# Kernel optimization log

Measured on AMD Instinct MI355X. Metric: run time of the kernel, lower is better.

Reference implementation:

```python
import jax, jax.numpy as jnp
import numpy as np

N = 100000      # nodes
E = 1600000     # edges
D_IN, D_H, D_OUT = 256, 64, 47


def setup_inputs() -> dict:
    key = jax.random.key(0)
    k0, k1, k2, k3 = jax.random.split(key, 4)
    x = jax.random.normal(k0, (N, D_IN), dtype=jnp.float32)
    edge_index = jax.random.randint(k1, (2, E), 0, N, dtype=jnp.int64)
    W1 = jax.random.normal(k2, (D_IN, D_H), dtype=jnp.float32) / np.sqrt(D_IN)
    b1 = jnp.zeros((D_H,), dtype=jnp.float32)
    W2 = jax.random.normal(k3, (D_H, D_OUT), dtype=jnp.float32) / np.sqrt(D_H)
    b2 = jnp.zeros((D_OUT,), dtype=jnp.float32)
    return {"x": x, "edge_index": edge_index, "W1": W1, "b1": b1, "W2": W2, "b2": b2}


def _gcn_conv(x, W, b, src, dst, norm):
    # PyG GCNConv: h = x @ W, then scatter_add(norm * h[src] -> dst), + bias
    h = x @ W                                     # [N, out]
    msg = norm[:, None] * h[src]                  # [E+N, out] gather
    out = jax.ops.segment_sum(msg, dst, num_segments=N)  # scatter-add
    return out + b


def reference(x, edge_index, W1, b1, W2, b2):
    # add self-loops with weight 1 (PyG default, edge_weight=None -> ones)
    loop = jnp.arange(N, dtype=edge_index.dtype)
    src = jnp.concatenate([edge_index[0], loop])
    dst = jnp.concatenate([edge_index[1], loop])
    w = jnp.ones((E + N,), dtype=x.dtype)
    # symmetric normalization: deg^-1/2[src] * w * deg^-1/2[dst]
    deg = jax.ops.segment_sum(w, dst, num_segments=N)
    dinv = jnp.where(deg > 0, jax.lax.rsqrt(deg), 0.0)
    norm = dinv[src] * w * dinv[dst]              # [E+N]

    h = _gcn_conv(x, W1, b1, src, dst, norm)
    h = jax.nn.relu(h)
    # F.dropout(training=self.training): eval mode -> identity
    xo = _gcn_conv(h, W2, b2, src, dst, norm)     # [N, D_OUT]
    logits = jax.nn.softmax(xo, axis=1)           # nn.Softmax() -> dim=1 for 2D
    preds = jnp.argmax(logits, axis=1)
    return (logits, preds, xo)
```

## Files before the change

kernel.cpp:

```cpp
#include <hip/hip_runtime.h>
#include <math.h>

#define NN 100000
#define NE 1600000
#define DI 256
#define DH 64
#define DO 47
#define DH3 48
#define PAD 48
#define RSZ8 ((NN + 7) / 8)
#define EPB 2048
#define CPB ((NE + EPB - 1) / EPB)

__global__ __launch_bounds__(256) void k_fill1(const int* __restrict__ src,
                                               const int* __restrict__ dst,
                                               int* __restrict__ deg,
                                               int* __restrict__ csr_pad) {
    int r = blockIdx.x & 7;
    int chunk = blockIdx.x >> 3;
    int lo = r * RSZ8, hi = min(lo + RSZ8, NN);
    int base = chunk * EPB + threadIdx.x;
    int dv[8];
    #pragma unroll
    for (int i = 0; i < 8; ++i) {
        int e = base + i * 256;
        dv[i] = (e < NE) ? __builtin_nontemporal_load(dst + e) : -1;
    }
    #pragma unroll
    for (int i = 0; i < 8; ++i) {
        int d = dv[i];
        if (d >= lo && d < hi) {
            int e = base + i * 256;
            int s = __builtin_nontemporal_load(src + e);
            int p = atomicAdd(&deg[d], 1);
            if (p < PAD) csr_pad[d * PAD + p] = s;
        }
    }
}

__global__ __launch_bounds__(512) void k_gemm1(const float* __restrict__ x,
                                               const float* __restrict__ W1,
                                               const int* __restrict__ deg,
                                               float* __restrict__ h1s) {
    __shared__ float xs[2][128 * 33];
    __shared__ float wl[2][32 * 64];
    const int t = threadIdx.x;
    const int lane = t & 63;
    const int wvu = __builtin_amdgcn_readfirstlane(t >> 6);
    const int r0 = blockIdx.x * 128;
    const int sr = t >> 2;
    const int sk = (t & 3) * 8;
    const int wk = t >> 4;
    const int wc = (t & 15) * 4;
    const long xrow = (long)min(r0 + sr, NN - 1) * DI;
    const int rowA = r0 + lane;
    const int rowB = r0 + 64 + lane;

    float accA[8] = {0.f, 0.f, 0.f, 0.f, 0.f, 0.f, 0.f, 0.f};
    float accB[8] = {0.f, 0.f, 0.f, 0.f, 0.f, 0.f, 0.f, 0.f};

    {
        float4 v0 = *(const float4*)(x + xrow + sk);
        float4 v1 = *(const float4*)(x + xrow + sk + 4);
        float* p = &xs[0][sr * 33 + sk];
        p[0] = v0.x; p[1] = v0.y; p[2] = v0.z; p[3] = v0.w;
        p[4] = v1.x; p[5] = v1.y; p[6] = v1.z; p[7] = v1.w;
        float4 w = *(const float4*)(W1 + (size_t)wk * DH + wc);
        float* q = &wl[0][wk * 64 + wc];
        q[0] = w.x; q[1] = w.y; q[2] = w.z; q[3] = w.w;
    }
    __syncthreads();
    for (int c = 0; c < 8; ++c) {
        const int buf = c & 1;
        if (c + 1 < 8) {
            float4 v0 = *(const float4*)(x + xrow + (c + 1) * 32 + sk);
            float4 v1 = *(const float4*)(x + xrow + (c + 1) * 32 + sk + 4);
            float* p = &xs[buf ^ 1][sr * 33 + sk];
            p[0] = v0.x; p[1] = v0.y; p[2] = v0.z; p[3] = v0.w;
            p[4] = v1.x; p[5] = v1.y; p[6] = v1.z; p[7] = v1.w;
            float4 w = *(const float4*)(W1 + (size_t)((c + 1) * 32 + wk) * DH + wc);
            float* q = &wl[buf ^ 1][wk * 64 + wc];
            q[0] = w.x; q[1] = w.y; q[2] = w.z; q[3] = w.w;
        }
        #pragma unroll 4
        for (int kk = 0; kk < 32; ++kk) {
            float xa = xs[buf][lane * 33 + kk];
            float xb = xs[buf][(lane + 64) * 33 + kk];
            const float4* wp = (const float4*)&wl[buf][kk * 64 + wvu * 8];
            float4 wa = wp[0], wb = wp[1];
            accA[0] += wa.x * xa; accA[1] += wa.y * xa;
            accA[2] += wa.z * xa; accA[3] += wa.w * xa;
            accA[4] += wb.x * xa; accA[5] += wb.y * xa;
            accA[6] += wb.z * xa; accA[7] += wb.w * xa;
            accB[0] += wa.x * xb; accB[1] += wa.y * xb;
            accB[2] += wa.z * xb; accB[3] += wa.w * xb;
            accB[4] += wb.x * xb; accB[5] += wb.y * xb;
            accB[6] += wb.z * xb; accB[7] += wb.w * xb;
        }
        __syncthreads();
    }
    if (rowA < NN) {
        float di = rsqrtf((float)(deg[rowA] + 1));
        float4 o0 = {di * accA[0], di * accA[1], di * accA[2], di * accA[3]};
        float4 o1 = {di * accA[4], di * accA[5], di * accA[6], di * accA[7]};
        float4* hp = (float4*)(h1s + (long)rowA * DH + wvu * 8);
        hp[0] = o0;
        hp[1] = o1;
    }
    if (rowB < NN) {
        float di = rsqrtf((float)(deg[rowB] + 1));
        float4 o0 = {di * accB[0], di * accB[1], di * accB[2], di * accB[3]};
        float4 o1 = {di * accB[4], di * accB[5], di * accB[6], di * accB[7]};
        float4* hp = (float4*)(h1s + (long)rowB * DH + wvu * 8);
        hp[0] = o0;
        hp[1] = o1;
    }
}

__global__ __launch_bounds__(256) void k_agg1(const int* __restrict__ deg,
                                              const int* __restrict__ csr_pad,
                                              const float* __restrict__ h1s,
                                              const float* __restrict__ b1,
                                              const float* __restrict__ W2,
                                              float* __restrict__ h3s) {
    __shared__ float w2[DH * DO];
    __shared__ float sh[8][DH];
    for (int i = threadIdx.x; i < DH * DO; i += 256) w2[i] = W2[i];
    __syncthreads();
    const int wv = threadIdx.x >> 6, lane = threadIdx.x & 63;
    const int c = lane & 15, e = lane >> 4;
    const unsigned c4 = (unsigned)(c * 4);
    const int rA = blockIdx.x * 8 + wv * 2, rB = rA + 1;
    const int degA = deg[rA], degB = deg[rB];
    const int cntA = min(degA, PAD), cntB = min(degB, PAD);
    const unsigned baseA = (unsigned)rA * PAD, baseB = (unsigned)rB * PAD;
    float aAx = 0.f, aAy = 0.f, aAz = 0.f, aAw = 0.f;
    float aBx = 0.f, aBy = 0.f, aBz = 0.f, aBw = 0.f;
    const int cmin = min(cntA, cntB), tmax = max(cntA, cntB);
    int j = 0;
    for (; j + 7 < cmin; j += 8) {
        unsigned sa0 = (unsigned)csr_pad[baseA + j + e];
        unsigned sb0 = (unsigned)csr_pad[baseB + j + e];
        unsigned sa1 = (unsigned)csr_pad[baseA + j + 4 + e];
        unsigned sb1 = (unsigned)csr_pad[baseB + j + 4 + e];
        float4 va0 = *(const float4*)(h1s + sa0 * 64u + c4);
        float4 vb0 = *(const float4*)(h1s + sb0 * 64u + c4);
        float4 va1 = *(const float4*)(h1s + sa1 * 64u + c4);
        float4 vb1 = *(const float4*)(h1s + sb1 * 64u + c4);
        aAx += va0.x + va1.x; aAy += va0.y + va1.y;
        aAz += va0.z + va1.z; aAw += va0.w + va1.w;
        aBx += vb0.x + vb1.x; aBy += vb0.y + vb1.y;
        aBz += vb0.z + vb1.z; aBw += vb0.w + vb1.w;
    }
    for (; j < tmax; j += 4) {
        int slot = min(j + e, PAD - 1);
        unsigned sa = min((unsigned)csr_pad[baseA + slot], (unsigned)(NN - 1));
        unsigned sb = min((unsigned)csr_pad[baseB + slot], (unsigned)(NN - 1));
        float4 va = *(const float4*)(h1s + sa * 64u + c4);
        float4 vb = *(const float4*)(h1s + sb * 64u + c4);
        float mA = (j + e < cntA) ? 1.f : 0.f;
        float mB = (j + e < cntB) ? 1.f : 0.f;
        aAx = fmaf(mA, va.x, aAx); aAy = fmaf(mA, va.y, aAy);
        aAz = fmaf(mA, va.z, aAz); aAw = fmaf(mA, va.w, aAw);
        aBx = fmaf(mB, vb.x, aBx); aBy = fmaf(mB, vb.y, aBy);
        aBz = fmaf(mB, vb.z, aBz); aBw = fmaf(mB, vb.w, aBw);
    }
    aAx += __shfl_xor(aAx, 16); aAx += __shfl_xor(aAx, 32);
    aAy += __shfl_xor(aAy, 16); aAy += __shfl_xor(aAy, 32);
    aAz += __shfl_xor(aAz, 16); aAz += __shfl_xor(aAz, 32);
    aAw += __shfl_xor(aAw, 16); aAw += __shfl_xor(aAw, 32);
    aBx += __shfl_xor(aBx, 16); aBx += __shfl_xor(aBx, 32);
    aBy += __shfl_xor(aBy, 16); aBy += __shfl_xor(aBy, 32);
    aBz += __shfl_xor(aBz, 16); aBz += __shfl_xor(aBz, 32);
    aBw += __shfl_xor(aBw, 16); aBw += __shfl_xor(aBw, 32);
    const float diA = rsqrtf((float)(degA + 1));
    const float diB = rsqrtf((float)(degB + 1));
    if (lane < 16) {
        float4 sA = *(const float4*)(h1s + (unsigned)rA * 64u + c4);
        float4 sB = *(const float4*)(h1s + (unsigned)rB * 64u + c4);
        float4 bb = *(const float4*)(b1 + c4);
        float4 oA, oB;
        oA.x = fmaxf(diA * (aAx + sA.x) + bb.x, 0.f);
        oA.y = fmaxf(diA * (aAy + sA.y) + bb.y, 0.f);
        oA.z = fmaxf(diA * (aAz + sA.z) + bb.z, 0.f);
        oA.w = fmaxf(diA * (aAw + sA.w) + bb.w, 0.f);
        oB.x = fmaxf(diB * (aBx + sB.x) + bb.x, 0.f);
        oB.y = fmaxf(diB * (aBy + sB.y) + bb.y, 0.f);
        oB.z = fmaxf(diB * (aBz + sB.z) + bb.z, 0.f);
        oB.w = fmaxf(diB * (aBw + sB.w) + bb.w, 0.f);
        *(float4*)&sh[wv * 2 + 0][c4] = oA;
        *(float4*)&sh[wv * 2 + 1][c4] = oB;
    }
    __syncthreads();
    if (lane < DO) {
        float oA = 0.f, oB = 0.f;
        #pragma unroll 8
        for (int k = 0; k < DH; ++k) {
            float w = w2[k * DO + lane];
            oA += sh[wv * 2 + 0][k] * w;
            oB += sh[wv * 2 + 1][k] * w;
        }
        h3s[(unsigned)rA * DH3 + lane] = diA * oA;
        h3s[(unsigned)rB * DH3 + lane] = diB * oB;
    }
}

__global__ __launch_bounds__(256) void k_agg2(const int* __restrict__ deg,
                                              const int* __restrict__ csr_pad,
                                              const float* __restrict__ h3s,
                                              const float* __restrict__ b2,
                                              float* __restrict__ logits,
                                              float* __restrict__ preds,
                                              float* __restrict__ xo) {
    const int wv = threadIdx.x >> 6, lane = threadIdx.x & 63;
    const int c = lane & 15, e = lane >> 4;
    const unsigned cc4 = (unsigned)(((c < 12) ? c : 0) * 4);
    const int rA = blockIdx.x * 8 + wv * 2, rB = rA + 1;
    const int degA = deg[rA], degB = deg[rB];
    const int cntA = min(degA, PAD), cntB = min(degB, PAD);
    const unsigned baseA = (unsigned)rA * PAD, baseB = (unsigned)rB * PAD;
    float aAx = 0.f, aAy = 0.f, aAz = 0.f, aAw = 0.f;
    float aBx = 0.f, aBy = 0.f, aBz = 0.f, aBw = 0.f;
    const int cmin = min(cntA, cntB), tmax = max(cntA, cntB);
    int j = 0;
    for (; j + 7 < cmin; j += 8) {
        unsigned sa0 = (unsigned)csr_pad[baseA + j + e];
        unsigned sb0 = (unsigned)csr_pad[baseB + j + e];
        unsigned sa1 = (unsigned)csr_pad[baseA + j + 4 + e];
        unsigned sb1 = (unsigned)csr_pad[baseB + j + 4 + e];
        float4 va0 = *(const float4*)(h3s + sa0 * 48u + cc4);
        float4 vb0 = *(const float4*)(h3s + sb0 * 48u + cc4);
        float4 va1 = *(const float4*)(h3s + sa1 * 48u + cc4);
        float4 vb1 = *(const float4*)(h3s + sb1 * 48u + cc4);
        aAx += va0.x + va1.x; aAy += va0.y + va1.y;
        aAz += va0.z + va1.z; aAw += va0.w + va1.w;
        aBx += vb0.x + vb1.x; aBy += vb0.y + vb1.y;
        aBz += vb0.z + vb1.z; aBw += vb0.w + vb1.w;
    }
    for (; j < tmax; j += 4) {
        int slot = min(j + e, PAD - 1);
        unsigned sa = min((unsigned)csr_pad[baseA + slot], (unsigned)(NN - 1));
        unsigned sb = min((unsigned)csr_pad[baseB + slot], (unsigned)(NN - 1));
        float4 va = *(const float4*)(h3s + sa * 48u + cc4);
        float4 vb = *(const float4*)(h3s + sb * 48u + cc4);
        float mA = (j + e < cntA) ? 1.f : 0.f;
        float mB = (j + e < cntB) ? 1.f : 0.f;
        aAx = fmaf(mA, va.x, aAx); aAy = fmaf(mA, va.y, aAy);
        aAz = fmaf(mA, va.z, aAz); aAw = fmaf(mA, va.w, aAw);
        aBx = fmaf(mB, vb.x, aBx); aBy = fmaf(mB, vb.y, aBy);
        aBz = fmaf(mB, vb.z, aBz); aBw = fmaf(mB, vb.w, aBw);
    }
    aAx += __shfl_xor(aAx, 16); aAx += __shfl_xor(aAx, 32);
    aAy += __shfl_xor(aAy, 16); aAy += __shfl_xor(aAy, 32);
    aAz += __shfl_xor(aAz, 16); aAz += __shfl_xor(aAz, 32);
    aAw += __shfl_xor(aAw, 16); aAw += __shfl_xor(aAw, 32);
    aBx += __shfl_xor(aBx, 16); aBx += __shfl_xor(aBx, 32);
    aBy += __shfl_xor(aBy, 16); aBy += __shfl_xor(aBy, 32);
    aBz += __shfl_xor(aBz, 16); aBz += __shfl_xor(aBz, 32);
    aBw += __shfl_xor(aBw, 16); aBw += __shfl_xor(aBw, 32);
    const float diA = rsqrtf((float)(degA + 1));
    const float diB = rsqrtf((float)(degB + 1));
    const bool lv = (lane < 16) && (c < 12);
    float b0 = 0.f, bq1 = 0.f, bq2 = 0.f, bq3 = 0.f;
    if (lv) {
        b0 = b2[c * 4 + 0]; bq1 = b2[c * 4 + 1]; bq2 = b2[c * 4 + 2];
        bq3 = (c < 11) ? b2[c * 4 + 3] : 0.f;
    }
    #pragma unroll
    for (int rr = 0; rr < 2; ++rr) {
        const int row = rr ? rB : rA;
        const float di = rr ? diB : diA;
        float ax = rr ? aBx : aAx, ay = rr ? aBy : aAy;
        float az = rr ? aBz : aAz, aw = rr ? aBw : aAw;
        float vx = -INFINITY, vy = -INFINITY, vz = -INFINITY, vw = -INFINITY;
        if (lv) {
            float4 sf = *(const float4*)(h3s + (unsigned)row * 48u + cc4);
            vx = di * (ax + sf.x) + b0;
            vy = di * (ay + sf.y) + bq1;
            vz = di * (az + sf.z) + bq2;
            vw = (c < 11) ? (di * (aw + sf.w) + bq3) : -INFINITY;
            float* xp = xo + (size_t)row * DO + c * 4;
            xp[0] = vx; xp[1] = vy; xp[2] = vz;
            if (c < 11) xp[3] = vw;
        }
        float lm = fmaxf(fmaxf(vx, vy), fmaxf(vz, vw));
        float gm = lm;
        for (int off = 32; off; off >>= 1) gm = fmaxf(gm, __shfl_xor(gm, off));
        int cand = 1 << 30;
        if (lv) {
            if (vx == gm) cand = c * 4 + 0;
            else if (vy == gm) cand = c * 4 + 1;
            else if (vz == gm) cand = c * 4 + 2;
            else if (c < 11 && vw == gm) cand = c * 4 + 3;
        }
        for (int off = 32; off; off >>= 1) cand = min(cand, __shfl_xor(cand, off));
        float e0 = 0.f, e1 = 0.f, e2 = 0.f, e3 = 0.f;
        if (lv) {
            e0 = expf(vx - gm); e1 = expf(vy - gm); e2 = expf(vz - gm);
            e3 = (c < 11) ? expf(vw - gm) : 0.f;
        }
        float gs = e0 + e1 + e2 + e3;
        for (int off = 32; off; off >>= 1) gs += __shfl_xor(gs, off);
        if (lv) {
            float* lp = logits + (size_t)row * DO + c * 4;
            lp[0] = e0 / gs; lp[1] = e1 / gs; lp[2] = e2 / gs;
            if (c < 11) lp[3] = e3 / gs;
        }
        if (lane == 0) preds[row] = (float)cand;
    }
}

extern "C" void kernel_launch(void* const* d_in, const int* in_sizes, int n_in,
                              void* d_out, int out_size, void* d_ws, size_t ws_size,
                              hipStream_t stream) {
    const float* x  = (const float*)d_in[0];
    const int*   ei = (const int*)d_in[1];
    const float* W1 = (const float*)d_in[2];
    const float* b1 = (const float*)d_in[3];
    const float* W2 = (const float*)d_in[4];
    const float* b2 = (const float*)d_in[5];
    const int* src = ei;
    const int* dst = ei + NE;

    float* out    = (float*)d_out;
    float* logits = out;
    float* preds  = out + (size_t)NN * DO;
    float* xo     = preds + NN;

    char* wsb = (char*)d_ws;
    int*   deg     = (int*)wsb;                         wsb += (size_t)NN * 4;
    int*   csr_pad = (int*)wsb;                         wsb += (size_t)NN * PAD * 4;
    float* h1s     = (float*)wsb;                       wsb += (size_t)NN * DH * 4;
    float* h3s     = (float*)wsb;                       wsb += (size_t)NN * DH3 * 4;

    hipMemsetAsync(deg, 0, NN * sizeof(int), stream);

    k_fill1<<<8 * CPB, 256, 0, stream>>>(src, dst, deg, csr_pad);
    k_gemm1<<<(NN + 127) / 128, 512, 0, stream>>>(x, W1, deg, h1s);
    k_agg1<<<NN / 8, 256, 0, stream>>>(deg, csr_pad, h1s, b1, W2, h3s);
    k_agg2<<<NN / 8, 256, 0, stream>>>(deg, csr_pad, h3s, b2, logits, preds, xo);
}
```

Before: 298.3 us.

## Fuse CSR fill with first GEMM in one interleaved launch; defer degree scaling

```diff
diff --git a/kernel.cpp b/kernel.cpp
--- a/kernel.cpp
+++ b/kernel.cpp
@@ -11,43 +11,51 @@
 #define RSZ8 ((NN + 7) / 8)
 #define EPB 2048
 #define CPB ((NE + EPB - 1) / EPB)
-
-__global__ __launch_bounds__(256) void k_fill1(const int* __restrict__ src,
+#define GNB ((NN + 127) / 128)
+#define FNB (GNB * 9)
+
+__global__ __launch_bounds__(512) void k_fused(const int* __restrict__ src,
                                                const int* __restrict__ dst,
+                                               const float* __restrict__ x,
+                                               const float* __restrict__ W1,
                                                int* __restrict__ deg,
-                                               int* __restrict__ csr_pad) {
-    int r = blockIdx.x & 7;
-    int chunk = blockIdx.x >> 3;
-    int lo = r * RSZ8, hi = min(lo + RSZ8, NN);
-    int base = chunk * EPB + threadIdx.x;
-    int dv[8];
-    #pragma unroll
-    for (int i = 0; i < 8; ++i) {
-        int e = base + i * 256;
-        dv[i] = (e < NE) ? __builtin_nontemporal_load(dst + e) : -1;
-    }
-    #pragma unroll
-    for (int i = 0; i < 8; ++i) {
-        int d = dv[i];
-        if (d >= lo && d < hi) {
-            int e = base + i * 256;
-            int s = __builtin_nontemporal_load(src + e);
-            int p = atomicAdd(&deg[d], 1);
-            if (p < PAD) csr_pad[d * PAD + p] = s;
-        }
-    }
-}
-
-__global__ __launch_bounds__(512) void k_gemm1(const float* __restrict__ x,
-                                               const float* __restrict__ W1,
-                                               const int* __restrict__ deg,
-                                               float* __restrict__ h1s) {
+                                               int* __restrict__ csr_pad,
+                                               float* __restrict__ h1u) {
     __shared__ float xs[2][128 * 33];
     __shared__ float wl[2][32 * 64];
+    const int b = blockIdx.x;
     const int t = threadIdx.x;
+
+    if (b % 9 != 0) {
+        const int r = b & 7;
+        const int k = ((b % 72) - r) >> 3;
+        const int ordinal = k - (k > r ? 1 : 0);
+        const int chunk = (b / 72) * 8 + ordinal;
+        const int lo = r * RSZ8, hi = min(lo + RSZ8, NN);
+        const int base = chunk * EPB + t;
+        int dv[4];
+        #pragma unroll
+        for (int i = 0; i < 4; ++i) {
+            int e = base + i * 512;
+            dv[i] = (e < NE) ? __builtin_nontemporal_load(dst + e) : -1;
+        }
+        #pragma unroll
+        for (int i = 0; i < 4; ++i) {
+            int d = dv[i];
+            if (d >= lo && d < hi) {
+                int e = base + i * 512;
+                int s = __builtin_nontemporal_load(src + e);
+                int p = atomicAdd(&deg[d], 1);
+                if (p < PAD) csr_pad[d * PAD + p] = s;
+            }
+        }
+        return;
+    }
+
+    const int g = b / 9;
     const int lane = t & 63;
     const int wvu = __builtin_amdgcn_readfirstlane(t >> 6);
-    const int r0 = blockIdx.x * 128;
+    const int r0 = g * 128;
     const int sr = t >> 2;
     const int sk = (t & 3) * 8;
     const int wk = t >> 4;
@@ -100,26 +108,31 @@
         __syncthreads();
     }
     if (rowA < NN) {
-        float di = rsqrtf((float)(deg[rowA] + 1));
-        float4 o0 = {di * accA[0], di * accA[1], di * accA[2], di * accA[3]};
-        float4 o1 = {di * accA[4], di * accA[5], di * accA[6], di * accA[7]};
-        float4* hp = (float4*)(h1s + (long)rowA * DH + wvu * 8);
+        float4 o0 = {accA[0], accA[1], accA[2], accA[3]};
+        float4 o1 = {accA[4], accA[5], accA[6], accA[7]};
+        float4* hp = (float4*)(h1u + (long)rowA * DH + wvu * 8);
         hp[0] = o0;
         hp[1] = o1;
     }
     if (rowB < NN) {
-        float di = rsqrtf((float)(deg[rowB] + 1));
-        float4 o0 = {di * accB[0], di * accB[1], di * accB[2], di * accB[3]};
-        float4 o1 = {di * accB[4], di * accB[5], di * accB[6], di * accB[7]};
-        float4* hp = (float4*)(h1s + (long)rowB * DH + wvu * 8);
+        float4 o0 = {accB[0], accB[1], accB[2], accB[3]};
+        float4 o1 = {accB[4], accB[5], accB[6], accB[7]};
+        float4* hp = (float4*)(h1u + (long)rowB * DH + wvu * 8);
         hp[0] = o0;
         hp[1] = o1;
     }
 }
 
+__global__ __launch_bounds__(256) void k_dinv(const int* __restrict__ deg,
+                                              float* __restrict__ dinv) {
+    int i = blockIdx.x * 256 + threadIdx.x;
+    if (i < NN) dinv[i] = rsqrtf((float)(deg[i] + 1));
+}
+
 __global__ __launch_bounds__(256) void k_agg1(const int* __restrict__ deg,
+                                              const float* __restrict__ dinv,
                                               const int* __restrict__ csr_pad,
-                                              const float* __restrict__ h1s,
+                                              const float* __restrict__ h1u,
                                               const float* __restrict__ b1,
                                               const float* __restrict__ W2,
                                               float* __restrict__ h3s) {
@@ -131,8 +144,7 @@
     const int c = lane & 15, e = lane >> 4;
     const unsigned c4 = (unsigned)(c * 4);
     const int rA = blockIdx.x * 8 + wv * 2, rB = rA + 1;
-    const int degA = deg[rA], degB = deg[rB];
-    const int cntA = min(degA, PAD), cntB = min(degB, PAD);
+    const int cntA = min(deg[rA], PAD), cntB = min(deg[rB], PAD);
     const unsigned baseA = (unsigned)rA * PAD, baseB = (unsigned)rB * PAD;
     float aAx = 0.f, aAy = 0.f, aAz = 0.f, aAw = 0.f;
     float aBx = 0.f, aBy = 0.f, aBz = 0.f, aBw = 0.f;
@@ -143,27 +155,32 @@
         unsigned sb0 = (unsigned)csr_pad[baseB + j + e];
         unsigned sa1 = (unsigned)csr_pad[baseA + j + 4 + e];
         unsigned sb1 = (unsigned)csr_pad[baseB + j + 4 + e];
-        float4 va0 = *(const float4*)(h1s + sa0 * 64u + c4);
-        float4 vb0 = *(const float4*)(h1s + sb0 * 64u + c4);
-        float4 va1 = *(const float4*)(h1s + sa1 * 64u + c4);
-        float4 vb1 = *(const float4*)(h1s + sb1 * 64u + c4);
-        aAx += va0.x + va1.x; aAy += va0.y + va1.y;
-        aAz += va0.z + va1.z; aAw += va0.w + va1.w;
-        aBx += vb0.x + vb1.x; aBy += vb0.y + vb1.y;
-        aBz += vb0.z + vb1.z; aBw += vb0.w + vb1.w;
+        float da0 = dinv[sa0], db0 = dinv[sb0], da1 = dinv[sa1], db1 = dinv[sb1];
+        float4 va0 = *(const float4*)(h1u + sa0 * 64u + c4);
+        float4 vb0 = *(const float4*)(h1u + sb0 * 64u + c4);
+        float4 va1 = *(const float4*)(h1u + sa1 * 64u + c4);
+        float4 vb1 = *(const float4*)(h1u + sb1 * 64u + c4);
+        aAx = fmaf(da0, va0.x, fmaf(da1, va1.x, aAx));
+        aAy = fmaf(da0, va0.y, fmaf(da1, va1.y, aAy));
+        aAz = fmaf(da0, va0.z, fmaf(da1, va1.z, aAz));
+        aAw = fmaf(da0, va0.w, fmaf(da1, va1.w, aAw));
+        aBx = fmaf(db0, vb0.x, fmaf(db1, vb1.x, aBx));
+        aBy = fmaf(db0, vb0.y, fmaf(db1, vb1.y, aBy));
+        aBz = fmaf(db0, vb0.z, fmaf(db1, vb1.z, aBz));
+        aBw = fmaf(db0, vb0.w, fmaf(db1, vb1.w, aBw));
     }
     for (; j < tmax; j += 4) {
         int slot = min(j + e, PAD - 1);
         unsigned sa = min((unsigned)csr_pad[baseA + slot], (unsigned)(NN - 1));
         unsigned sb = min((unsigned)csr_pad[baseB + slot], (unsigned)(NN - 1));
-        float4 va = *(const float4*)(h1s + sa * 64u + c4);
-        float4 vb = *(const float4*)(h1s + sb * 64u + c4);
-        float mA = (j + e < cntA) ? 1.f : 0.f;
-        float mB = (j + e < cntB) ? 1.f : 0.f;
-        aAx = fmaf(mA, va.x, aAx); aAy = fmaf(mA, va.y, aAy);
-        aAz = fmaf(mA, va.z, aAz); aAw = fmaf(mA, va.w, aAw);
-        aBx = fmaf(mB, vb.x, aBx); aBy = fmaf(mB, vb.y, aBy);
-        aBz = fmaf(mB, vb.z, aBz); aBw = fmaf(mB, vb.w, aBw);
+        float4 va = *(const float4*)(h1u + sa * 64u + c4);
+        float4 vb = *(const float4*)(h1u + sb * 64u + c4);
+        float wA = ((j + e < cntA) ? 1.f : 0.f) * dinv[sa];
+        float wB = ((j + e < cntB) ? 1.f : 0.f) * dinv[sb];
+        aAx = fmaf(wA, va.x, aAx); aAy = fmaf(wA, va.y, aAy);
+        aAz = fmaf(wA, va.z, aAz); aAw = fmaf(wA, va.w, aAw);
+        aBx = fmaf(wB, vb.x, aBx); aBy = fmaf(wB, vb.y, aBy);
+        aBz = fmaf(wB, vb.z, aBz); aBw = fmaf(wB, vb.w, aBw);
     }
     aAx += __shfl_xor(aAx, 16); aAx += __shfl_xor(aAx, 32);
     aAy += __shfl_xor(aAy, 16); aAy += __shfl_xor(aAy, 32);
@@ -173,21 +190,20 @@
     aBy += __shfl_xor(aBy, 16); aBy += __shfl_xor(aBy, 32);
     aBz += __shfl_xor(aBz, 16); aBz += __shfl_xor(aBz, 32);
     aBw += __shfl_xor(aBw, 16); aBw += __shfl_xor(aBw, 32);
-    const float diA = rsqrtf((float)(degA + 1));
-    const float diB = rsqrtf((float)(degB + 1));
+    const float diA = dinv[rA], diB = dinv[rB];
     if (lane < 16) {
-        float4 sA = *(const float4*)(h1s + (unsigned)rA * 64u + c4);
-        float4 sB = *(const float4*)(h1s + (unsigned)rB * 64u + c4);
+        float4 sA = *(const float4*)(h1u + (unsigned)rA * 64u + c4);
+        float4 sB = *(const float4*)(h1u + (unsigned)rB * 64u + c4);
         float4 bb = *(const float4*)(b1 + c4);
         float4 oA, oB;
-        oA.x = fmaxf(diA * (aAx + sA.x) + bb.x, 0.f);
-        oA.y = fmaxf(diA * (aAy + sA.y) + bb.y, 0.f);
-        oA.z = fmaxf(diA * (aAz + sA.z) + bb.z, 0.f);
-        oA.w = fmaxf(diA * (aAw + sA.w) + bb.w, 0.f);
-        oB.x = fmaxf(diB * (aBx + sB.x) + bb.x, 0.f);
-        oB.y = fmaxf(diB * (aBy + sB.y) + bb.y, 0.f);
-        oB.z = fmaxf(diB * (aBz + sB.z) + bb.z, 0.f);
-        oB.w = fmaxf(diB * (aBw + sB.w) + bb.w, 0.f);
+        oA.x = fmaxf(diA * (aAx + diA * sA.x) + bb.x, 0.f);
+        oA.y = fmaxf(diA * (aAy + diA * sA.y) + bb.y, 0.f);
+        oA.z = fmaxf(diA * (aAz + diA * sA.z) + bb.z, 0.f);
+        oA.w = fmaxf(diA * (aAw + diA * sA.w) + bb.w, 0.f);
+        oB.x = fmaxf(diB * (aBx + diB * sB.x) + bb.x, 0.f);
+        oB.y = fmaxf(diB * (aBy + diB * sB.y) + bb.y, 0.f);
+        oB.z = fmaxf(diB * (aBz + diB * sB.z) + bb.z, 0.f);
+        oB.w = fmaxf(diB * (aBw + diB * sB.w) + bb.w, 0.f);
         *(float4*)&sh[wv * 2 + 0][c4] = oA;
         *(float4*)&sh[wv * 2 + 1][c4] = oB;
     }
@@ -329,14 +345,15 @@
 
     char* wsb = (char*)d_ws;
     int*   deg     = (int*)wsb;                         wsb += (size_t)NN * 4;
+    float* dinv    = (float*)wsb;                       wsb += (size_t)NN * 4;
     int*   csr_pad = (int*)wsb;                         wsb += (size_t)NN * PAD * 4;
-    float* h1s     = (float*)wsb;                       wsb += (size_t)NN * DH * 4;
+    float* h1u     = (float*)wsb;                       wsb += (size_t)NN * DH * 4;
     float* h3s     = (float*)wsb;                       wsb += (size_t)NN * DH3 * 4;
 
     hipMemsetAsync(deg, 0, NN * sizeof(int), stream);
 
-    k_fill1<<<8 * CPB, 256, 0, stream>>>(src, dst, deg, csr_pad);
-    k_gemm1<<<(NN + 127) / 128, 512, 0, stream>>>(x, W1, deg, h1s);
-    k_agg1<<<NN / 8, 256, 0, stream>>>(deg, csr_pad, h1s, b1, W2, h3s);
+    k_fused<<<FNB, 512, 0, stream>>>(src, dst, x, W1, deg, csr_pad, h1u);
+    k_dinv<<<(NN + 255) / 256, 256, 0, stream>>>(deg, dinv);
+    k_agg1<<<NN / 8, 256, 0, stream>>>(deg, dinv, csr_pad, h1u, b1, W2, h3s);
     k_agg2<<<NN / 8, 256, 0, stream>>>(deg, csr_pad, h3s, b2, logits, preds, xo);
 }
```

New measurement: 289.7 us. 1.03x faster.
